# Kernel optimization log

Hardware: AMD Instinct MI355X
Metric: run time of the kernel (lower is better)

The kernel has to match this reference:

```python
import jax, jax.numpy as jnp
import numpy as np
from jax import lax

FILTERS = 64

def _conv(a, k):
    # NHWC input, HWIO kernel, SAME padding, stride 1
    return lax.conv_general_dilated(a, k, window_strides=(1, 1), padding='SAME',
                                    dimension_numbers=('NHWC', 'HWIO', 'NHWC'))

def _hard_sigmoid(z):
    # Keras ConvLSTM2D default recurrent_activation
    return jnp.clip(0.2 * z + 0.5, 0.0, 1.0)

def setup_inputs() -> dict:
    key = jax.random.key(0)
    k1, k2, k3 = jax.random.split(key, 3)
    B, T, H, W, C = 8, 16, 96, 96, 8
    x = jax.random.normal(k1, (B, T, H, W, C), dtype=jnp.float32)
    Wx = jax.random.normal(k2, (3, 3, C, 4 * FILTERS), dtype=jnp.float32) * 0.05
    Wh = jax.random.normal(k3, (3, 3, FILTERS, 4 * FILTERS), dtype=jnp.float32) * 0.05
    b = jnp.zeros((4 * FILTERS,), dtype=jnp.float32)
    return {"x": x, "Wx": Wx, "Wh": Wh, "b": b}

def reference(x, Wx, Wh, b):
    # Keras ConvLSTM2D forward (inference: dropout off), return_sequences=False.
    B, T, H, W, C = x.shape
    F = Wh.shape[2]

    def step(carry, xt):
        h, c = carry
        z = _conv(xt, Wx) + _conv(h, Wh) + b  # (B,H,W,4F)
        i, f, g, o = jnp.split(z, 4, axis=-1)  # Keras gate order i,f,c,o
        i = _hard_sigmoid(i)
        f = _hard_sigmoid(f)
        o = _hard_sigmoid(o)
        c_new = f * c + i * jnp.tanh(g)
        h_new = o * jnp.tanh(c_new)
        return (h_new, c_new), None

    h0 = jnp.zeros((B, H, W, F), x.dtype)
    xs = jnp.moveaxis(x, 1, 0)  # (T,B,H,W,C)
    (h, c), _ = lax.scan(step, (h0, h0), xs)
    return h  # (B,H,W,F)
```

## Files before the change

### kernel.cpp

```cpp
#include <hip/hip_runtime.h>
#include <cmath>


#define HTOT 96
#define WTOT 96
#define CINX 8
#define FF   64
#define G4   256
#define BB   8
#define TT   16
#define NPOS (BB*HTOT*WTOT)

typedef __attribute__((ext_vector_type(8))) short short8;
typedef __attribute__((ext_vector_type(4))) float floatx4;

union U16 { uint4 u; short8 s; };

__device__ __forceinline__ float hsig(float z) {
    return fminf(fmaxf(0.2f * z + 0.5f, 0.f), 1.f);
}

__device__ __forceinline__ float ftanh(float x) {
    float e = __expf(-2.f * fabsf(x));
    float t = (1.f - e) / (1.f + e);
    return copysignf(t, x);
}

__device__ __forceinline__ ushort f2bf(float f) {
    unsigned u = __float_as_uint(f);
    u = (u + 0x7fff + ((u >> 16) & 1)) >> 16;
    return (ushort)u;
}

__device__ __forceinline__ void async16(const void* g, void* l) {
    __builtin_amdgcn_global_load_lds(
        (const __attribute__((address_space(1))) void*)g,
        (__attribute__((address_space(3))) void*)l, 16, 0, 0);
}

__global__ __launch_bounds__(256) void conv_x_bf16(const float* __restrict__ x,
                                                   ushort* __restrict__ xbf, int n4) {
    int i = blockIdx.x * 256 + threadIdx.x;
    if (i >= n4) return;
    float4 v = ((const float4*)x)[i];
    ushort4 o;
    o.x = f2bf(v.x); o.y = f2bf(v.y); o.z = f2bf(v.z); o.w = f2bf(v.w);
    ((ushort4*)xbf)[i] = o;
}

__global__ __launch_bounds__(256) void prep_w(const float* __restrict__ Wx,
                                              const float* __restrict__ Wh,
                                              ushort* __restrict__ Bp) {
    int idx = blockIdx.x * 256 + threadIdx.x;
    if (idx >= 4 * 21 * 256) return;
    int lane = idx & 63;
    int g = (idx >> 6) & 3;
    int rest = idx >> 8;
    int s = rest % 21, slice = rest / 21;
    int q = lane >> 4, col = lane & 15;
    int n = g * 64 + slice * 16 + col;
    ushort o[8];
    if (s < 18) {
        int dxw = s / 6, rem = s - 6 * dxw;
        int khw = rem / 3, dyw = rem - 3 * khw;
        int tap = dyw * 3 + dxw;
        int cbase = khw * 32 + q * 8;
        #pragma unroll
        for (int j = 0; j < 8; ++j)
            o[j] = f2bf(Wh[((size_t)tap * FF + cbase + j) * G4 + n]);
    } else {
        int tap = (s - 18) * 4 + q;
        #pragma unroll
        for (int j = 0; j < 8; ++j)
            o[j] = (tap < 9) ? f2bf(Wx[((size_t)tap * CINX + j) * G4 + n]) : (ushort)0;
    }
    U16 u;
    #pragma unroll
    for (int j = 0; j < 8; ++j) ((ushort*)&u)[j] = o[j];
    ((uint4*)Bp)[idx] = u.u;
}

__global__ __launch_bounds__(256, 4) void convlstm_mfma(
    const ushort* __restrict__ xbf, int t,
    const ushort* __restrict__ hS_in,
    ushort* __restrict__ hS_out,
    float* __restrict__ cS,
    const ushort* __restrict__ Bp,
    const float* __restrict__ bias,
    const uint4* __restrict__ zpad,
    float* __restrict__ out, int last)
{
    __shared__ __align__(16) ushort hplanes[8 * 2048];
    __shared__ __align__(16) ushort xplane[2048];
    __shared__ __align__(16) uint4  bslab[3 * 256];

    const int tid = threadIdx.x;
    const int x0 = blockIdx.x * 16, y0 = blockIdx.y * 12;
    const int bb = blockIdx.z >> 2, slice = blockIdx.z & 3;

    const uint4* gB = (const uint4*)Bp + (size_t)(slice * 21) * 256 + tid;
    async16(gB,       &bslab[tid]);
    async16(gB + 256, &bslab[256 + tid]);

    {
        int py = tid / 18, px = tid - py * 18;
        int gy = y0 - 1 + py, gx = x0 - 1 + px;
        bool ok = (gy >= 0 && gy < HTOT && gx >= 0 && gx < WTOT);
        int gyc = gy < 0 ? 0 : (gy > HTOT - 1 ? HTOT - 1 : gy);
        int gxc = gx < 0 ? 0 : (gx > WTOT - 1 ? WTOT - 1 : gx);
        size_t gpos = ((size_t)bb * HTOT + gyc) * WTOT + gxc;
        #pragma unroll
        for (int p = 0; p < 8; ++p) {
            const void* src = ok
                ? (const void*)(hS_in + ((size_t)(p >> 1) * NPOS + gpos) * 16 + (p & 1) * 8)
                : (const void*)zpad;
            async16(src, hplanes + p * 2048 + tid * 8);
        }
        const void* sxp = ok
            ? (const void*)(xbf + ((((size_t)bb * TT + t) * HTOT + gyc) * WTOT + gxc) * CINX)
            : (const void*)zpad;
        async16(sxp, xplane + tid * 8);
    }

    const int w = tid >> 6, lane = tid & 63, q = lane >> 4, col = lane & 15;
    const int rowb = w * 3;

    const ushort* hA = hplanes + q * 2048 + (rowb * 18 + col) * 8;
    const uint4*  bA = bslab + lane;

    floatx4 acc[3][4];
    #pragma unroll
    for (int g = 0; g < 4; ++g) {
        float bv = bias[g * 64 + slice * 16 + col];
        acc[0][g] = (floatx4){bv, bv, bv, bv};
        acc[1][g] = (floatx4){bv, bv, bv, bv};
        acc[2][g] = (floatx4){bv, bv, bv, bv};
    }

    __syncthreads();

    U16 aw[4];
    #pragma unroll
    for (int dx = 0; dx < 3; ++dx) {
        #pragma unroll
        for (int kh = 0; kh < 2; ++kh) {
            #pragma unroll
            for (int j = 0; j < 3; ++j)
                aw[j].u = *(const uint4*)(hA + kh * 8192 + j * 144 + dx * 8);
            #pragma unroll
            for (int dy = 0; dy < 3; ++dy) {
                const int s = dx * 6 + kh * 3 + dy;
                if (dy)
                    aw[(dy + 2) & 3].u = *(const uint4*)(hA + kh * 8192 + (dy + 2) * 144 + dx * 8);
                async16(gB + (s + 2) * 256, &bslab[((dy + 2) % 3) * 256 + tid]);
                #pragma unroll
                for (int g = 0; g < 4; ++g) {
                    U16 b4; b4.u = bA[dy * 256 + g * 64];
                    #pragma unroll
                    for (int mt = 0; mt < 3; ++mt)
                        acc[mt][g] = __builtin_amdgcn_mfma_f32_16x16x32_bf16(
                            aw[(mt + dy) & 3].s, b4.s, acc[mt][g], 0, 0, 0);
                }
                asm volatile("s_waitcnt vmcnt(1)" ::: "memory");
                __builtin_amdgcn_s_barrier();
                __builtin_amdgcn_sched_barrier(0);
            }
        }
    }
    #pragma unroll
    for (int sx = 0; sx < 3; ++sx) {
        int tap = sx * 4 + q; if (tap > 8) tap = 8;
        int dyq = tap / 3, dxq = tap - 3 * dyq;
        const ushort* xA = xplane + ((rowb + dyq) * 18 + col + dxq) * 8;
        if (sx == 0) async16(gB + 20 * 256, &bslab[2 * 256 + tid]);
        U16 a4[3];
        #pragma unroll
        for (int mt = 0; mt < 3; ++mt)
            a4[mt].u = *(const uint4*)(xA + mt * 144);
        #pragma unroll
        for (int g = 0; g < 4; ++g) {
            U16 b4; b4.u = bA[sx * 256 + g * 64];
            #pragma unroll
            for (int mt = 0; mt < 3; ++mt)
                acc[mt][g] = __builtin_amdgcn_mfma_f32_16x16x32_bf16(
                    a4[mt].s, b4.s, acc[mt][g], 0, 0, 0);
        }
        if (sx == 0) {
            asm volatile("s_waitcnt vmcnt(1)" ::: "memory");
            __builtin_amdgcn_s_barrier();
            __builtin_amdgcn_sched_barrier(0);
        } else if (sx == 1) {
            asm volatile("s_waitcnt vmcnt(0)" ::: "memory");
            __builtin_amdgcn_s_barrier();
            __builtin_amdgcn_sched_barrier(0);
        }
    }

    #pragma unroll
    for (int mt = 0; mt < 3; ++mt) {
        int gy = y0 + rowb + mt;
        #pragma unroll
        for (int r = 0; r < 4; ++r) {
            int gx = x0 + q * 4 + r;
            size_t gpos = ((size_t)bb * HTOT + gy) * WTOT + gx;
            size_t idx = ((size_t)slice * NPOS + gpos) * 16 + col;
            float zi = acc[mt][0][r], zf = acc[mt][1][r];
            float zg = acc[mt][2][r], zo = acc[mt][3][r];
            float cn = hsig(zf) * cS[idx] + hsig(zi) * ftanh(zg);
            cS[idx] = cn;
            float hn = hsig(zo) * ftanh(cn);
            hS_out[idx] = f2bf(hn);
            if (last) out[gpos * 64 + slice * 16 + col] = hn;
        }
    }
}

extern "C" void kernel_launch(void* const* d_in, const int* in_sizes, int n_in,
                              void* d_out, int out_size, void* d_ws, size_t ws_size,
                              hipStream_t stream) {
    const float* x  = (const float*)d_in[0];
    const float* Wx = (const float*)d_in[1];
    const float* Wh = (const float*)d_in[2];
    const float* b  = (const float*)d_in[3];

    const size_t NX = (size_t)BB * TT * HTOT * WTOT * CINX;
    const size_t NH = (size_t)NPOS * FF;

    char* ws = (char*)d_ws;
    ushort* xbf = (ushort*)ws;                  ws += NX * 2;
    ushort* hS0 = (ushort*)ws;                  ws += NH * 2;
    ushort* hS1 = (ushort*)ws;                  ws += NH * 2;
    float*  cS  = (float*)ws;                   ws += NH * 4;
    ushort* Bp  = (ushort*)ws;                  ws += (size_t)4*21*256*16;
    uint4*  zpad = (uint4*)ws;

    hipMemsetAsync(hS0, 0, NH * 2, stream);
    hipMemsetAsync(cS,  0, NH * 4, stream);
    hipMemsetAsync(zpad, 0, 64, stream);

    conv_x_bf16<<<(int)((NX / 4 + 255) / 256), 256, 0, stream>>>(x, xbf, (int)(NX / 4));
    prep_w<<<(4 * 21 * 256 + 255) / 256, 256, 0, stream>>>(Wx, Wh, Bp);

    dim3 grid(WTOT / 16, HTOT / 12, BB * 4);
    for (int t = 0; t < TT; ++t) {
        const ushort* hin = (t & 1) ? hS1 : hS0;
        ushort* hout      = (t & 1) ? hS0 : hS1;
        convlstm_mfma<<<grid, 256, 0, stream>>>(xbf, t, hin, hout, cS, Bp, b, zpad,
                                                (float*)d_out, t == TT - 1);
    }
}
```

Baseline: 587.7 us.

## Load weight slabs directly into registers with double buffering, dropping LDS ring

Removes the shared-memory ring that staged the packed weight slab per filter tap. Each wave now reads its B fragments straight from global memory into a two-deep register buffer, prefetching the next tap while the current one feeds MFMAs. This eliminates the per-tap s_waitcnt plus workgroup barrier, which serialized the four waves. In exchange, each wave fetches the same weights redundantly through the cache hierarchy, global load latency is exposed more directly, and register pressure rises under the 4-blocks-per-CU launch bound.

```diff
diff --git a/kernel.cpp b/kernel.cpp
--- a/kernel.cpp
+++ b/kernel.cpp
@@ -92,15 +92,15 @@
 {
     __shared__ __align__(16) ushort hplanes[8 * 2048];
     __shared__ __align__(16) ushort xplane[2048];
-    __shared__ __align__(16) uint4  bslab[3 * 256];
 
     const int tid = threadIdx.x;
     const int x0 = blockIdx.x * 16, y0 = blockIdx.y * 12;
     const int bb = blockIdx.z >> 2, slice = blockIdx.z & 3;
 
-    const uint4* gB = (const uint4*)Bp + (size_t)(slice * 21) * 256 + tid;
-    async16(gB,       &bslab[tid]);
-    async16(gB + 256, &bslab[256 + tid]);
+    const int w = tid >> 6, lane = tid & 63, q = lane >> 4, col = lane & 15;
+    const int rowb = w * 3;
+
+    const uint4* gB = (const uint4*)Bp + (size_t)(slice * 21) * 256 + lane;
 
     {
         int py = tid / 18, px = tid - py * 18;
@@ -122,11 +122,11 @@
         async16(sxp, xplane + tid * 8);
     }
 
-    const int w = tid >> 6, lane = tid & 63, q = lane >> 4, col = lane & 15;
-    const int rowb = w * 3;
-
     const ushort* hA = hplanes + q * 2048 + (rowb * 18 + col) * 8;
-    const uint4*  bA = bslab + lane;
+
+    U16 bbuf[2][4];
+    #pragma unroll
+    for (int g = 0; g < 4; ++g) bbuf[0][g].u = gB[g * 64];
 
     floatx4 acc[3][4];
     #pragma unroll
@@ -150,50 +150,41 @@
             #pragma unroll
             for (int dy = 0; dy < 3; ++dy) {
                 const int s = dx * 6 + kh * 3 + dy;
+                #pragma unroll
+                for (int g = 0; g < 4; ++g)
+                    bbuf[(s + 1) & 1][g].u = gB[(s + 1) * 256 + g * 64];
                 if (dy)
                     aw[(dy + 2) & 3].u = *(const uint4*)(hA + kh * 8192 + (dy + 2) * 144 + dx * 8);
-                async16(gB + (s + 2) * 256, &bslab[((dy + 2) % 3) * 256 + tid]);
                 #pragma unroll
-                for (int g = 0; g < 4; ++g) {
-                    U16 b4; b4.u = bA[dy * 256 + g * 64];
+                for (int g = 0; g < 4; ++g)
                     #pragma unroll
                     for (int mt = 0; mt < 3; ++mt)
                         acc[mt][g] = __builtin_amdgcn_mfma_f32_16x16x32_bf16(
-                            aw[(mt + dy) & 3].s, b4.s, acc[mt][g], 0, 0, 0);
-                }
-                asm volatile("s_waitcnt vmcnt(1)" ::: "memory");
-                __builtin_amdgcn_s_barrier();
-                __builtin_amdgcn_sched_barrier(0);
+                            aw[(mt + dy) & 3].s, bbuf[s & 1][g].s, acc[mt][g], 0, 0, 0);
             }
         }
     }
     #pragma unroll
     for (int sx = 0; sx < 3; ++sx) {
+        const int s = 18 + sx;
         int tap = sx * 4 + q; if (tap > 8) tap = 8;
         int dyq = tap / 3, dxq = tap - 3 * dyq;
         const ushort* xA = xplane + ((rowb + dyq) * 18 + col + dxq) * 8;
-        if (sx == 0) async16(gB + 20 * 256, &bslab[2 * 256 + tid]);
+        if (sx < 2) {
+            #pragma unroll
+            for (int g = 0; g < 4; ++g)
+                bbuf[(s + 1) & 1][g].u = gB[(s + 1) * 256 + g * 64];
+        }
         U16 a4[3];
         #pragma unroll
         for (int mt = 0; mt < 3; ++mt)
             a4[mt].u = *(const uint4*)(xA + mt * 144);
         #pragma unroll
-        for (int g = 0; g < 4; ++g) {
-            U16 b4; b4.u = bA[sx * 256 + g * 64];
+        for (int g = 0; g < 4; ++g)
             #pragma unroll
             for (int mt = 0; mt < 3; ++mt)
                 acc[mt][g] = __builtin_amdgcn_mfma_f32_16x16x32_bf16(
-                    a4[mt].s, b4.s, acc[mt][g], 0, 0, 0);
-        }
-        if (sx == 0) {
-            asm volatile("s_waitcnt vmcnt(1)" ::: "memory");
-            __builtin_amdgcn_s_barrier();
-            __builtin_amdgcn_sched_barrier(0);
-        } else if (sx == 1) {
-            asm volatile("s_waitcnt vmcnt(0)" ::: "memory");
-            __builtin_amdgcn_s_barrier();
-            __builtin_amdgcn_sched_barrier(0);
-        }
+                    a4[mt].s, bbuf[s & 1][g].s, acc[mt][g], 0, 0, 0);
     }
 
     #pragma unroll
```

Result: no change. 588.3 us (+0.1%).
